# Optimization experiments

Measured on AMD Instinct MI355X. Metric: run time of the kernel, lower is better.

## Reference

```python
import jax, jax.numpy as jnp
import numpy as np

NUM_HEADS = 16
HEAD_DIM = 64
EPS = 1e-6


def rms_norm(x, w):
    # normalize in float32, cast back (matches torch RMSNorm.forward)
    xf = x.astype(jnp.float32)
    y = xf * jax.lax.rsqrt(jnp.mean(xf * xf, axis=-1, keepdims=True) + EPS)
    return y.astype(x.dtype) * w


def setup_inputs() -> dict:
    key = jax.random.key(0)
    ks = jax.random.split(key, 5)
    B, N, C = 2, 2048, 1024
    x = jax.random.normal(ks[0], (B, N, C), dtype=jnp.float32)
    w_qkv = jax.random.normal(ks[1], (3 * C, C), dtype=jnp.float32) * (1.0 / np.sqrt(C))
    b_qkv = jax.random.normal(ks[2], (3 * C,), dtype=jnp.float32) * 0.02
    q_norm_w = jnp.ones((HEAD_DIM,), dtype=jnp.float32)
    k_norm_w = jnp.ones((HEAD_DIM,), dtype=jnp.float32)
    w_proj = jax.random.normal(ks[3], (C, C), dtype=jnp.float32) * (1.0 / np.sqrt(C))
    b_proj = jax.random.normal(ks[4], (C,), dtype=jnp.float32) * 0.02
    return {"x": x, "w_qkv": w_qkv, "b_qkv": b_qkv, "q_norm_w": q_norm_w,
            "k_norm_w": k_norm_w, "w_proj": w_proj, "b_proj": b_proj}


def reference(x, w_qkv, b_qkv, q_norm_w, k_norm_w, w_proj, b_proj):
    B, N, C = x.shape
    H, D = NUM_HEADS, HEAD_DIM
    scale = D ** -0.5
    # fused QKV projection: [B,N,3C]
    qkv = jnp.einsum('bnc,oc->bno', x, w_qkv) + b_qkv
    qkv = qkv.reshape(B, N, 3, H, D)
    q = qkv[:, :, 0].transpose(0, 2, 1, 3)  # [B,H,N,D]
    k = qkv[:, :, 1].transpose(0, 2, 1, 3)
    v = qkv[:, :, 2].transpose(0, 2, 1, 3)
    q = rms_norm(q, q_norm_w)
    k = rms_norm(k, k_norm_w)
    # SDPA (no causal mask, no dropout)
    scores = jnp.einsum('bhqd,bhkd->bhqk', q, k) * scale
    attn = jax.nn.softmax(scores, axis=-1)
    out = jnp.einsum('bhqk,bhkd->bhqd', attn, v)  # [B,H,N,D]
    out = out.transpose(0, 2, 1, 3).reshape(B, N, C)
    return jnp.einsum('bnc,oc->bno', out, w_proj) + b_proj
```

## Files before the change

### kernel.cpp

```cpp
#include <hip/hip_runtime.h>
#include <hip/hip_bf16.h>

typedef __attribute__((ext_vector_type(8))) short short8;
typedef __attribute__((ext_vector_type(8))) unsigned short ushort8;
typedef __attribute__((ext_vector_type(4))) float f32x4;
typedef __attribute__((ext_vector_type(4))) unsigned short u16x4;

#define MFMA16(a, b, c) __builtin_amdgcn_mfma_f32_16x16x32_bf16(a, b, c, 0, 0, 0)

__device__ __forceinline__ unsigned short f2bf(float f) {
  union { float f; unsigned u; } x; x.f = f;
  unsigned r = x.u + 0x7FFFu + ((x.u >> 16) & 1u);
  return (unsigned short)(r >> 16);
}
__device__ __forceinline__ float bf2f(unsigned short h) {
  union { unsigned u; float f; } x; x.u = ((unsigned)h) << 16;
  return x.f;
}
__device__ __forceinline__ void load_lds16(const void* g, void* l) {
  __builtin_amdgcn_global_load_lds((const __attribute__((address_space(1))) void*)g,
                                   (__attribute__((address_space(3))) void*)l, 16, 0, 0);
}

__global__ __launch_bounds__(256) void convert_all(
    const float* __restrict__ x, const float* __restrict__ wqkv, const float* __restrict__ wproj,
    unsigned short* __restrict__ xb, unsigned short* __restrict__ wqkvb,
    unsigned short* __restrict__ wprojb) {
  int i = blockIdx.x * 256 + threadIdx.x;
  const float4* src; unsigned short* dst; int o;
  if (i < 1048576) { src = (const float4*)x; dst = xb; o = i; }
  else if (i < 1048576 + 786432) { src = (const float4*)wqkv; dst = wqkvb; o = i - 1048576; }
  else { src = (const float4*)wproj; dst = wprojb; o = i - (1048576 + 786432); }
  float4 v = src[o];
  u16x4 r; r.x = f2bf(v.x); r.y = f2bf(v.y); r.z = f2bf(v.z); r.w = f2bf(v.w);
  *(u16x4*)(dst + (size_t)o * 4) = r;
}

template <bool OUT_BF16>
__global__ __launch_bounds__(256) void gemm_nt(
    const unsigned short* __restrict__ A, const unsigned short* __restrict__ Bm,
    const float* __restrict__ bias, void* __restrict__ Cout, int M, int N, int K) {
  __shared__ unsigned short As[128 * 32];
  __shared__ unsigned short Bs[128 * 32];
  const int t = threadIdx.x, w = t >> 6, l = t & 63;
  const int la = l & 15, lg = l >> 4;
  const int wm = w >> 1, wn = w & 1;
  const int m0 = blockIdx.y * 128, n0 = blockIdx.x * 128;

  const int r0 = t >> 2, c0 = (t & 3) ^ ((r0 >> 1) & 3);
  const int r1 = r0 + 64, c1 = (t & 3) ^ ((r1 >> 1) & 3);
  const unsigned short* a0 = A + (size_t)(m0 + r0) * K + c0 * 8;
  const unsigned short* a1 = A + (size_t)(m0 + r1) * K + c1 * 8;
  const unsigned short* b0 = Bm + (size_t)(n0 + r0) * K + c0 * 8;
  const unsigned short* b1 = Bm + (size_t)(n0 + r1) * K + c1 * 8;
  char* ldsA0 = (char*)As + w * 1024;
  char* ldsA1 = (char*)As + w * 1024 + 4096;
  char* ldsB0 = (char*)Bs + w * 1024;
  char* ldsB1 = (char*)Bs + w * 1024 + 4096;

  f32x4 acc[4][4] = {};
  int offA[4], offB[4];
#pragma unroll
  for (int f = 0; f < 4; ++f) {
    int ra = wm * 64 + f * 16 + la;
    offA[f] = ra * 64 + ((lg ^ ((ra >> 1) & 3)) * 16);
    int rb = wn * 64 + f * 16 + la;
    offB[f] = rb * 64 + ((lg ^ ((rb >> 1) & 3)) * 16);
  }

  for (int kt = 0; kt < K; kt += 32) {
    __syncthreads();
    load_lds16(a0 + kt, ldsA0);
    load_lds16(a1 + kt, ldsA1);
    load_lds16(b0 + kt, ldsB0);
    load_lds16(b1 + kt, ldsB1);
    __syncthreads();
    short8 af[4], bf[4];
#pragma unroll
    for (int f = 0; f < 4; ++f) af[f] = *(const short8*)((const char*)As + offA[f]);
#pragma unroll
    for (int f = 0; f < 4; ++f) bf[f] = *(const short8*)((const char*)Bs + offB[f]);
#pragma unroll
    for (int mf = 0; mf < 4; ++mf)
#pragma unroll
      for (int nf = 0; nf < 4; ++nf)
        acc[mf][nf] = MFMA16(af[mf], bf[nf], acc[mf][nf]);
  }

  const int colb = n0 + wn * 64 + la;
  const int rowb = m0 + wm * 64 + lg * 4;
#pragma unroll
  for (int nf = 0; nf < 4; ++nf) {
    const int col = colb + nf * 16;
    const float bv = bias[col];
#pragma unroll
    for (int mf = 0; mf < 4; ++mf)
#pragma unroll
      for (int r = 0; r < 4; ++r) {
        const int row = rowb + mf * 16 + r;
        float v = acc[mf][nf][r] + bv;
        if (OUT_BF16)
          ((unsigned short*)Cout)[(size_t)row * N + col] = f2bf(v);
        else
          ((float*)Cout)[(size_t)row * N + col] = v;
      }
  }
}

__global__ __launch_bounds__(256) void rmsnorm_qk(
    unsigned short* __restrict__ qkv, const float* __restrict__ qw, const float* __restrict__ kw) {
  const int t = threadIdx.x, w = t >> 6, l = t & 63;
  const int row = blockIdx.x * 32 + w * 8 + (l >> 3);
  const int part = row >> 16;
  const int rem = row & 65535;
  const int bn = rem >> 4, h = rem & 15;
  unsigned short* p = qkv + (size_t)bn * 3072 + part * 1024 + h * 64 + (l & 7) * 8;
  ushort8 v = *(const ushort8*)p;
  float f[8]; float s = 0.f;
#pragma unroll
  for (int j = 0; j < 8; ++j) { f[j] = bf2f(v[j]); s += f[j] * f[j]; }
  s += __shfl_xor(s, 1); s += __shfl_xor(s, 2); s += __shfl_xor(s, 4);
  const float r = rsqrtf(s * (1.f / 64.f) + 1e-6f);
  const float* nw = part ? kw : qw;
  ushort8 o;
#pragma unroll
  for (int j = 0; j < 8; ++j) o[j] = f2bf(f[j] * r * nw[(l & 7) * 8 + j]);
  *(ushort8*)p = o;
}

__global__ __launch_bounds__(256) void transpose_v(
    const unsigned short* __restrict__ qkv, unsigned short* __restrict__ vT) {
  __shared__ unsigned short tile[64][72];
  const int t = threadIdx.x;
  const int tn = blockIdx.x, bh = blockIdx.y;
  const int b = bh >> 4, h = bh & 15;
  for (int i = t; i < 512; i += 256) {
    const int n = i >> 3, c = i & 7;
    ushort8 v = *(const ushort8*)(qkv + (size_t)(b * 2048 + tn * 64 + n) * 3072 + 2048 + h * 64 + c * 8);
    *(ushort8*)&tile[n][c * 8] = v;
  }
  __syncthreads();
  for (int i = t; i < 512; i += 256) {
    const int d = i >> 3, c = i & 7;
    ushort8 o;
#pragma unroll
    for (int j = 0; j < 8; ++j) o[j] = tile[c * 8 + j][d];
    *(ushort8*)(vT + (size_t)(bh * 64 + d) * 2048 + tn * 64 + c * 8) = o;
  }
}

__global__ __launch_bounds__(256) void attn_fwd(
    const unsigned short* __restrict__ qkv, const unsigned short* __restrict__ vT,
    unsigned short* __restrict__ outb) {
  __shared__ unsigned short Ks[64 * 64];
  __shared__ unsigned short Vs[64 * 64];
  __shared__ unsigned short Ps[4][16][76];
  const int t = threadIdx.x, w = t >> 6, l = t & 63;
  const int la = l & 15, lg = l >> 4;
  const int q0 = blockIdx.x * 64, bh = blockIdx.y;
  const int b = bh >> 4, h = bh & 15;

  const int qrow = q0 + w * 16 + la;
  const unsigned short* qp = qkv + (size_t)(b * 2048 + qrow) * 3072 + h * 64;
  const short8 qa0 = *(const short8*)(qp + lg * 8);
  const short8 qa1 = *(const short8*)(qp + 32 + lg * 8);

  const int r0 = t >> 3, c0 = (t & 7) ^ (r0 & 7);
  const int r1 = r0 + 32, c1 = (t & 7) ^ (r1 & 7);
  const unsigned short* k0p = qkv + (size_t)(b * 2048 + r0) * 3072 + 1024 + h * 64 + c0 * 8;
  const unsigned short* k1p = qkv + (size_t)(b * 2048 + r1) * 3072 + 1024 + h * 64 + c1 * 8;
  const unsigned short* v0p = vT + (size_t)(bh * 64 + r0) * 2048 + c0 * 8;
  const unsigned short* v1p = vT + (size_t)(bh * 64 + r1) * 2048 + c1 * 8;

  f32x4 accO[4] = {};
  float lsum = 0.f;
  const float SC = 0.125f * 1.44269504f;
  const float M = 12.0f;

  for (int kb = 0; kb < 2048; kb += 64) {
    __syncthreads();
    load_lds16(k0p + (size_t)kb * 3072, (char*)Ks + w * 1024);
    load_lds16(k1p + (size_t)kb * 3072, (char*)Ks + w * 1024 + 4096);
    load_lds16(v0p + kb, (char*)Vs + w * 1024);
    load_lds16(v1p + kb, (char*)Vs + w * 1024 + 4096);
    __syncthreads();

    f32x4 s[4] = {};
#pragma unroll
    for (int nf = 0; nf < 4; ++nf) {
      const int kr = nf * 16 + la;
      const short8 kf0 = *(const short8*)((const char*)Ks + kr * 128 + ((lg ^ (kr & 7)) * 16));
      const short8 kf1 = *(const short8*)((const char*)Ks + kr * 128 + (((4 + lg) ^ (kr & 7)) * 16));
      s[nf] = MFMA16(kf0, qa0, s[nf]);
      s[nf] = MFMA16(kf1, qa1, s[nf]);
    }
#pragma unroll
    for (int nf = 0; nf < 4; ++nf) {
      float e[4];
#pragma unroll
      for (int r = 0; r < 4; ++r)
        e[r] = exp2f(__builtin_fmaf(s[nf][r], SC, -M));
      lsum += (e[0] + e[1]) + (e[2] + e[3]);
      union { __hip_bfloat162 h[2]; u16x4 v; } pk;
      pk.h[0] = __float22bfloat162_rn(float2{e[0], e[1]});
      pk.h[1] = __float22bfloat162_rn(float2{e[2], e[3]});
      *(u16x4*)&Ps[w][la][nf * 16 + lg * 4] = pk.v;
    }
    asm volatile("" ::: "memory");
    const short8 pa0 = *(const short8*)&Ps[w][la][lg * 8];
    const short8 pa1 = *(const short8*)&Ps[w][la][32 + lg * 8];

#pragma unroll
    for (int df = 0; df < 4; ++df) {
      const int vr = df * 16 + la;
      const short8 vf0 = *(const short8*)((const char*)Vs + vr * 128 + ((lg ^ (vr & 7)) * 16));
      const short8 vf1 = *(const short8*)((const char*)Vs + vr * 128 + (((4 + lg) ^ (vr & 7)) * 16));
      accO[df] = MFMA16(pa0, vf0, accO[df]);
      accO[df] = MFMA16(pa1, vf1, accO[df]);
    }
  }
  lsum += __shfl_xor(lsum, 16);
  lsum += __shfl_xor(lsum, 32);
#pragma unroll
  for (int r = 0; r < 4; ++r) {
    const float inv = 1.f / __shfl(lsum, lg * 4 + r);
    const int orow = q0 + w * 16 + lg * 4 + r;
    unsigned short* op = outb + (size_t)(b * 2048 + orow) * 1024 + h * 64 + la;
#pragma unroll
    for (int df = 0; df < 4; ++df) op[df * 16] = f2bf(accO[df][r] * inv);
  }
}

extern "C" void kernel_launch(void* const* d_in, const int* in_sizes, int n_in,
                              void* d_out, int out_size, void* d_ws, size_t ws_size,
                              hipStream_t stream) {
  const float* x     = (const float*)d_in[0];
  const float* wqkv  = (const float*)d_in[1];
  const float* bqkv  = (const float*)d_in[2];
  const float* qnw   = (const float*)d_in[3];
  const float* knw   = (const float*)d_in[4];
  const float* wproj = (const float*)d_in[5];
  const float* bproj = (const float*)d_in[6];

  char* p = (char*)d_ws;
  unsigned short* xb     = (unsigned short*)p; p += (size_t)4096 * 1024 * 2;
  unsigned short* wqkvb  = (unsigned short*)p; p += (size_t)3072 * 1024 * 2;
  unsigned short* wprojb = (unsigned short*)p; p += (size_t)1024 * 1024 * 2;
  unsigned short* qkvb   = (unsigned short*)p; p += (size_t)4096 * 3072 * 2;
  unsigned short* vT     = (unsigned short*)p; p += (size_t)32 * 64 * 2048 * 2;
  unsigned short* aout   = (unsigned short*)p; p += (size_t)4096 * 1024 * 2;

  convert_all<<<8192, 256, 0, stream>>>(x, wqkv, wproj, xb, wqkvb, wprojb);
  gemm_nt<true><<<dim3(24, 32), 256, 0, stream>>>(xb, wqkvb, bqkv, qkvb, 4096, 3072, 1024);
  rmsnorm_qk<<<4096, 256, 0, stream>>>(qkvb, qnw, knw);
  transpose_v<<<dim3(32, 32), 256, 0, stream>>>(qkvb, vT);
  attn_fwd<<<dim3(32, 32), 256, 0, stream>>>(qkvb, vT, aout);
  gemm_nt<false><<<dim3(8, 32), 256, 0, stream>>>(aout, wprojb, bproj, d_out, 4096, 1024, 1024);
}
```

Baseline: 151.7 us.

## Load two K/V tiles per barrier pair and XOR-swizzle the P scratch buffer

The attention loop now stages two 64-key K/V tiles into separate LDS buffers per iteration, which halves the number of __syncthreads pairs and puts more global-to-LDS loads in flight at once. The P staging buffer drops its padding in favour of an XOR swizzle on writes and reads to avoid bank conflicts. This doubles K/V LDS usage and may lower occupancy. There is still no overlap between loading and compute, because both tiles are waited on before either is used.

```diff
diff --git a/kernel.cpp b/kernel.cpp
--- a/kernel.cpp
+++ b/kernel.cpp
@@ -152,9 +152,9 @@
 __global__ __launch_bounds__(256) void attn_fwd(
     const unsigned short* __restrict__ qkv, const unsigned short* __restrict__ vT,
     unsigned short* __restrict__ outb) {
-  __shared__ unsigned short Ks[64 * 64];
-  __shared__ unsigned short Vs[64 * 64];
-  __shared__ unsigned short Ps[4][16][76];
+  __shared__ unsigned short Ks[2][64 * 64];
+  __shared__ unsigned short Vs[2][64 * 64];
+  __shared__ unsigned short Ps[4][16][64];
   const int t = threadIdx.x, w = t >> 6, l = t & 63;
   const int la = l & 15, lg = l >> 4;
   const int q0 = blockIdx.x * 64, bh = blockIdx.y;
@@ -177,23 +177,26 @@
   const float SC = 0.125f * 1.44269504f;
   const float M = 12.0f;
 
-  for (int kb = 0; kb < 2048; kb += 64) {
-    __syncthreads();
-    load_lds16(k0p + (size_t)kb * 3072, (char*)Ks + w * 1024);
-    load_lds16(k1p + (size_t)kb * 3072, (char*)Ks + w * 1024 + 4096);
-    load_lds16(v0p + kb, (char*)Vs + w * 1024);
-    load_lds16(v1p + kb, (char*)Vs + w * 1024 + 4096);
-    __syncthreads();
-
+  char* psBase = (char*)Ps + w * 2048 + la * 128;
+  const int swzW[4] = {
+      ((0 * 2 + (lg >> 1)) ^ (la & 7)) * 16 + (lg & 1) * 8,
+      ((1 * 2 + (lg >> 1)) ^ (la & 7)) * 16 + (lg & 1) * 8,
+      ((2 * 2 + (lg >> 1)) ^ (la & 7)) * 16 + (lg & 1) * 8,
+      ((3 * 2 + (lg >> 1)) ^ (la & 7)) * 16 + (lg & 1) * 8};
+  const int swzR0 = (lg ^ (la & 7)) * 16;
+  const int swzR1 = ((4 + lg) ^ (la & 7)) * 16;
+
+  auto computeTile = [&](const char* KsB, const char* VsB) {
     f32x4 s[4] = {};
 #pragma unroll
     for (int nf = 0; nf < 4; ++nf) {
       const int kr = nf * 16 + la;
-      const short8 kf0 = *(const short8*)((const char*)Ks + kr * 128 + ((lg ^ (kr & 7)) * 16));
-      const short8 kf1 = *(const short8*)((const char*)Ks + kr * 128 + (((4 + lg) ^ (kr & 7)) * 16));
+      const short8 kf0 = *(const short8*)(KsB + kr * 128 + ((lg ^ (kr & 7)) * 16));
+      const short8 kf1 = *(const short8*)(KsB + kr * 128 + (((4 + lg) ^ (kr & 7)) * 16));
       s[nf] = MFMA16(kf0, qa0, s[nf]);
       s[nf] = MFMA16(kf1, qa1, s[nf]);
     }
+    asm volatile("" ::: "memory");
 #pragma unroll
     for (int nf = 0; nf < 4; ++nf) {
       float e[4];
@@ -201,23 +204,37 @@
       for (int r = 0; r < 4; ++r)
         e[r] = exp2f(__builtin_fmaf(s[nf][r], SC, -M));
       lsum += (e[0] + e[1]) + (e[2] + e[3]);
-      union { __hip_bfloat162 h[2]; u16x4 v; } pk;
-      pk.h[0] = __float22bfloat162_rn(float2{e[0], e[1]});
-      pk.h[1] = __float22bfloat162_rn(float2{e[2], e[3]});
-      *(u16x4*)&Ps[w][la][nf * 16 + lg * 4] = pk.v;
+      union { __hip_bfloat162 hh[2]; u16x4 v; } pk;
+      pk.hh[0] = __float22bfloat162_rn(float2{e[0], e[1]});
+      pk.hh[1] = __float22bfloat162_rn(float2{e[2], e[3]});
+      *(u16x4*)(psBase + swzW[nf]) = pk.v;
     }
     asm volatile("" ::: "memory");
-    const short8 pa0 = *(const short8*)&Ps[w][la][lg * 8];
-    const short8 pa1 = *(const short8*)&Ps[w][la][32 + lg * 8];
-
+    const short8 pa0 = *(const short8*)(psBase + swzR0);
+    const short8 pa1 = *(const short8*)(psBase + swzR1);
 #pragma unroll
     for (int df = 0; df < 4; ++df) {
       const int vr = df * 16 + la;
-      const short8 vf0 = *(const short8*)((const char*)Vs + vr * 128 + ((lg ^ (vr & 7)) * 16));
-      const short8 vf1 = *(const short8*)((const char*)Vs + vr * 128 + (((4 + lg) ^ (vr & 7)) * 16));
+      const short8 vf0 = *(const short8*)(VsB + vr * 128 + ((lg ^ (vr & 7)) * 16));
+      const short8 vf1 = *(const short8*)(VsB + vr * 128 + (((4 + lg) ^ (vr & 7)) * 16));
       accO[df] = MFMA16(pa0, vf0, accO[df]);
       accO[df] = MFMA16(pa1, vf1, accO[df]);
     }
+  };
+
+  for (int kb = 0; kb < 2048; kb += 128) {
+    __syncthreads();
+    load_lds16(k0p + (size_t)kb * 3072, (char*)Ks[0] + w * 1024);
+    load_lds16(k1p + (size_t)kb * 3072, (char*)Ks[0] + w * 1024 + 4096);
+    load_lds16(v0p + kb, (char*)Vs[0] + w * 1024);
+    load_lds16(v1p + kb, (char*)Vs[0] + w * 1024 + 4096);
+    load_lds16(k0p + (size_t)(kb + 64) * 3072, (char*)Ks[1] + w * 1024);
+    load_lds16(k1p + (size_t)(kb + 64) * 3072, (char*)Ks[1] + w * 1024 + 4096);
+    load_lds16(v0p + kb + 64, (char*)Vs[1] + w * 1024);
+    load_lds16(v1p + kb + 64, (char*)Vs[1] + w * 1024 + 4096);
+    __syncthreads();
+    computeTile((const char*)Ks[0], (const char*)Vs[0]);
+    computeTile((const char*)Ks[1], (const char*)Vs[1]);
   }
   lsum += __shfl_xor(lsum, 16);
   lsum += __shfl_xor(lsum, 32);
```

Result: no change. 152.2 us (+0.3%).

## Fuse QK RMSNorm and V transpose into QKV GEMM epilogue

Applied to the files above, without the earlier changes.

The QKV GEMM epilogue now applies per-head RMSNorm to Q and K tiles in fp32 registers, using cross-lane shuffles to sum over the 64-wide head, and writes V directly in transposed layout. This removes the separate rmsnorm_qk and transpose_v kernels, along with their launches and extra passes over the qkv buffer. The attention kernel also switches exp2f to the hardware exp2 intrinsic. In exchange, the V stores are strided 8-byte writes, and normalizing before bf16 rounding changes numerics slightly.

```diff
diff --git a/kernel.cpp b/kernel.cpp
--- a/kernel.cpp
+++ b/kernel.cpp
@@ -36,10 +36,12 @@
   *(u16x4*)(dst + (size_t)o * 4) = r;
 }
 
-template <bool OUT_BF16>
+template <int MODE>
 __global__ __launch_bounds__(256) void gemm_nt(
     const unsigned short* __restrict__ A, const unsigned short* __restrict__ Bm,
-    const float* __restrict__ bias, void* __restrict__ Cout, int M, int N, int K) {
+    const float* __restrict__ bias, void* __restrict__ Cout, int M, int N, int K,
+    const float* __restrict__ qnw, const float* __restrict__ knw,
+    unsigned short* __restrict__ vT) {
   __shared__ unsigned short As[128 * 32];
   __shared__ unsigned short Bs[128 * 32];
   const int t = threadIdx.x, w = t >> 6, l = t & 63;
@@ -89,63 +91,74 @@
 
   const int colb = n0 + wn * 64 + la;
   const int rowb = m0 + wm * 64 + lg * 4;
+
 #pragma unroll
   for (int nf = 0; nf < 4; ++nf) {
-    const int col = colb + nf * 16;
-    const float bv = bias[col];
+    const float bv = bias[colb + nf * 16];
 #pragma unroll
     for (int mf = 0; mf < 4; ++mf)
 #pragma unroll
-      for (int r = 0; r < 4; ++r) {
-        const int row = rowb + mf * 16 + r;
-        float v = acc[mf][nf][r] + bv;
-        if (OUT_BF16)
-          ((unsigned short*)Cout)[(size_t)row * N + col] = f2bf(v);
-        else
-          ((float*)Cout)[(size_t)row * N + col] = v;
+      for (int r = 0; r < 4; ++r) acc[mf][nf][r] += bv;
+  }
+
+  if (MODE == 0) {
+#pragma unroll
+    for (int nf = 0; nf < 4; ++nf) {
+      const int col = colb + nf * 16;
+#pragma unroll
+      for (int mf = 0; mf < 4; ++mf)
+#pragma unroll
+        for (int r = 0; r < 4; ++r)
+          ((float*)Cout)[(size_t)(rowb + mf * 16 + r) * N + col] = acc[mf][nf][r];
+    }
+  } else {
+    const int part = n0 >> 10;
+    if (part < 2) {
+      const float* nw = part ? knw : qnw;
+      float nwv[4];
+#pragma unroll
+      for (int nf = 0; nf < 4; ++nf) nwv[nf] = nw[la + nf * 16];
+#pragma unroll
+      for (int mf = 0; mf < 4; ++mf)
+#pragma unroll
+        for (int r = 0; r < 4; ++r) {
+          float ss = acc[mf][0][r] * acc[mf][0][r];
+#pragma unroll
+          for (int nf = 1; nf < 4; ++nf) ss = __builtin_fmaf(acc[mf][nf][r], acc[mf][nf][r], ss);
+          ss += __shfl_xor(ss, 1); ss += __shfl_xor(ss, 2);
+          ss += __shfl_xor(ss, 4); ss += __shfl_xor(ss, 8);
+          const float rs = rsqrtf(ss * (1.f / 64.f) + 1e-6f);
+#pragma unroll
+          for (int nf = 0; nf < 4; ++nf) acc[mf][nf][r] *= rs * nwv[nf];
+        }
+    }
+    if (part < 2) {
+#pragma unroll
+      for (int nf = 0; nf < 4; ++nf) {
+        const int col = colb + nf * 16;
+#pragma unroll
+        for (int mf = 0; mf < 4; ++mf)
+#pragma unroll
+          for (int r = 0; r < 4; ++r)
+            ((unsigned short*)Cout)[(size_t)(rowb + mf * 16 + r) * N + col] = f2bf(acc[mf][nf][r]);
       }
-  }
-}
-
-__global__ __launch_bounds__(256) void rmsnorm_qk(
-    unsigned short* __restrict__ qkv, const float* __restrict__ qw, const float* __restrict__ kw) {
-  const int t = threadIdx.x, w = t >> 6, l = t & 63;
-  const int row = blockIdx.x * 32 + w * 8 + (l >> 3);
-  const int part = row >> 16;
-  const int rem = row & 65535;
-  const int bn = rem >> 4, h = rem & 15;
-  unsigned short* p = qkv + (size_t)bn * 3072 + part * 1024 + h * 64 + (l & 7) * 8;
-  ushort8 v = *(const ushort8*)p;
-  float f[8]; float s = 0.f;
-#pragma unroll
-  for (int j = 0; j < 8; ++j) { f[j] = bf2f(v[j]); s += f[j] * f[j]; }
-  s += __shfl_xor(s, 1); s += __shfl_xor(s, 2); s += __shfl_xor(s, 4);
-  const float r = rsqrtf(s * (1.f / 64.f) + 1e-6f);
-  const float* nw = part ? kw : qw;
-  ushort8 o;
-#pragma unroll
-  for (int j = 0; j < 8; ++j) o[j] = f2bf(f[j] * r * nw[(l & 7) * 8 + j]);
-  *(ushort8*)p = o;
-}
-
-__global__ __launch_bounds__(256) void transpose_v(
-    const unsigned short* __restrict__ qkv, unsigned short* __restrict__ vT) {
-  __shared__ unsigned short tile[64][72];
-  const int t = threadIdx.x;
-  const int tn = blockIdx.x, bh = blockIdx.y;
-  const int b = bh >> 4, h = bh & 15;
-  for (int i = t; i < 512; i += 256) {
-    const int n = i >> 3, c = i & 7;
-    ushort8 v = *(const ushort8*)(qkv + (size_t)(b * 2048 + tn * 64 + n) * 3072 + 2048 + h * 64 + c * 8);
-    *(ushort8*)&tile[n][c * 8] = v;
-  }
-  __syncthreads();
-  for (int i = t; i < 512; i += 256) {
-    const int d = i >> 3, c = i & 7;
-    ushort8 o;
-#pragma unroll
-    for (int j = 0; j < 8; ++j) o[j] = tile[c * 8 + j][d];
-    *(ushort8*)(vT + (size_t)(bh * 64 + d) * 2048 + tn * 64 + c * 8) = o;
+    } else {
+#pragma unroll
+      for (int nf = 0; nf < 4; ++nf) {
+        const int col = colb + nf * 16;
+        const int h = (col >> 6) & 15;
+        const int d = la + nf * 16;
+#pragma unroll
+        for (int mf = 0; mf < 4; ++mf) {
+          const int row = rowb + mf * 16;
+          const int b = row >> 11, n = row & 2047;
+          u16x4 o;
+#pragma unroll
+          for (int r = 0; r < 4; ++r) o[r] = f2bf(acc[mf][nf][r]);
+          *(u16x4*)(vT + ((size_t)(b * 16 + h) * 64 + d) * 2048 + n) = o;
+        }
+      }
+    }
   }
 }
 
@@ -199,11 +212,11 @@
       float e[4];
 #pragma unroll
       for (int r = 0; r < 4; ++r)
-        e[r] = exp2f(__builtin_fmaf(s[nf][r], SC, -M));
+        e[r] = __builtin_amdgcn_exp2f(__builtin_fmaf(s[nf][r], SC, -M));
       lsum += (e[0] + e[1]) + (e[2] + e[3]);
-      union { __hip_bfloat162 h[2]; u16x4 v; } pk;
-      pk.h[0] = __float22bfloat162_rn(float2{e[0], e[1]});
-      pk.h[1] = __float22bfloat162_rn(float2{e[2], e[3]});
+      union { __hip_bfloat162 hh[2]; u16x4 v; } pk;
+      pk.hh[0] = __float22bfloat162_rn(float2{e[0], e[1]});
+      pk.hh[1] = __float22bfloat162_rn(float2{e[2], e[3]});
       *(u16x4*)&Ps[w][la][nf * 16 + lg * 4] = pk.v;
     }
     asm volatile("" ::: "memory");
@@ -251,9 +264,9 @@
   unsigned short* aout   = (unsigned short*)p; p += (size_t)4096 * 1024 * 2;
 
   convert_all<<<8192, 256, 0, stream>>>(x, wqkv, wproj, xb, wqkvb, wprojb);
-  gemm_nt<true><<<dim3(24, 32), 256, 0, stream>>>(xb, wqkvb, bqkv, qkvb, 4096, 3072, 1024);
-  rmsnorm_qk<<<4096, 256, 0, stream>>>(qkvb, qnw, knw);
-  transpose_v<<<dim3(32, 32), 256, 0, stream>>>(qkvb, vT);
+  gemm_nt<1><<<dim3(24, 32), 256, 0, stream>>>(xb, wqkvb, bqkv, qkvb, 4096, 3072, 1024,
+                                               qnw, knw, vT);
   attn_fwd<<<dim3(32, 32), 256, 0, stream>>>(qkvb, vT, aout);
-  gemm_nt<false><<<dim3(8, 32), 256, 0, stream>>>(aout, wprojb, bproj, d_out, 4096, 1024, 1024);
-}
+  gemm_nt<0><<<dim3(8, 32), 256, 0, stream>>>(aout, wprojb, bproj, d_out, 4096, 1024, 1024,
+                                              nullptr, nullptr, nullptr);
+}
```

Result: faster. 131.6 us (-13.3%).
